# Kernel optimization log

Measured on AMD Instinct MI355X. Metric: run time of the kernel, lower is better.

Reference implementation:

```python
import jax, jax.numpy as jnp
import numpy as np

BATCH = 1
SEQ = 2048
HIDDEN = 2048
NUM_HEADS = 16
NUM_KV_HEADS = 4
HEAD_DIM = HIDDEN // NUM_HEADS  # 128
KV_GROUPS = NUM_HEADS // NUM_KV_HEADS  # 4
MIN_WIN, MAX_WIN = 64, 512


def _adaptive_window_mask(key):
    # Per-query adaptive window size in [MIN_WIN, MAX_WIN); causal + windowed.
    win = jax.random.randint(key, (SEQ,), MIN_WIN, MAX_WIN)  # [S]
    i = jnp.arange(SEQ)[:, None]  # query pos
    j = jnp.arange(SEQ)[None, :]  # key pos
    mask = (j <= i) & (j > i - win[:, None])  # diagonal always True
    return jnp.broadcast_to(mask[None, None], (BATCH, 1, SEQ, SEQ))


def setup_inputs() -> dict:
    key = jax.random.key(0)
    ks = jax.random.split(key, 6)
    std = 0.02
    return {
        "hidden_states": jax.random.normal(ks[0], (BATCH, SEQ, HIDDEN), jnp.float32),
        "attention_mask": _adaptive_window_mask(ks[1]),
        "Wq": jax.random.normal(ks[2], (HIDDEN, NUM_HEADS * HEAD_DIM), jnp.float32) * std,
        "Wk": jax.random.normal(ks[3], (HIDDEN, NUM_KV_HEADS * HEAD_DIM), jnp.float32) * std,
        "Wv": jax.random.normal(ks[4], (HIDDEN, NUM_KV_HEADS * HEAD_DIM), jnp.float32) * std,
        "Wo": jax.random.normal(ks[5], (NUM_HEADS * HEAD_DIM, HIDDEN), jnp.float32) * std,
    }


def reference(hidden_states, attention_mask, Wq, Wk, Wv, Wo):
    B, S, H = hidden_states.shape
    # Projections (no bias, LLaMA-style)
    q = (hidden_states @ Wq).reshape(B, S, NUM_HEADS, HEAD_DIM).transpose(0, 2, 1, 3)
    k = (hidden_states @ Wk).reshape(B, S, NUM_KV_HEADS, HEAD_DIM).transpose(0, 2, 1, 3)
    v = (hidden_states @ Wv).reshape(B, S, NUM_KV_HEADS, HEAD_DIM).transpose(0, 2, 1, 3)
    # GQA: repeat_interleave along head dim
    k = jnp.repeat(k, KV_GROUPS, axis=1)  # [B, NUM_HEADS, S, D]
    v = jnp.repeat(v, KV_GROUPS, axis=1)
    scale = 1.0 / np.sqrt(HEAD_DIM).astype(np.float32)
    scores = jnp.einsum("bhqd,bhkd->bhqk", q, k) * scale  # [B, H, S, S]
    # bool mask: masked positions get -inf (matches masked_fill_(-inf) + add)
    scores = jnp.where(attention_mask, scores, -jnp.inf)
    attn = jax.nn.softmax(scores, axis=-1)
    out = jnp.einsum("bhqk,bhkd->bhqd", attn, v)
    out = out.transpose(0, 2, 1, 3).reshape(B, S, H) @ Wo
    return out
```

## Files before the change

kernel.cpp:

```cpp
#include <hip/hip_runtime.h>
#include <hip/hip_bf16.h>

typedef __attribute__((ext_vector_type(4)))  float f32x4;
typedef __attribute__((ext_vector_type(16))) float f32x16;
typedef __attribute__((ext_vector_type(8)))  short bf16x8;
typedef unsigned short u16;
typedef unsigned int   u32;
typedef unsigned long long u64;
typedef __attribute__((ext_vector_type(2))) u32 u32x2;
typedef __attribute__((ext_vector_type(4))) u32 u32x4;

#define S_LEN 2048
#define HID   2048
#define NH    16
#define NKV   4
#define HD    128
#define DKV   512
#define QK_SCALE 0.08838834764831845f

__device__ __forceinline__ u16 f2bf(float x) {
    u32 u = __builtin_bit_cast(u32, x);
    u32 r = (u + 0x7fffu + ((u >> 16) & 1u)) >> 16;
    return (u16)r;
}
__device__ __forceinline__ float bf2f(u16 b) {
    u32 u = ((u32)b) << 16;
    return __builtin_bit_cast(float, u);
}
__device__ __forceinline__ void gload_lds16(const void* g, void* l) {
    __builtin_amdgcn_global_load_lds(
        (const __attribute__((address_space(1))) u32*)g,
        (__attribute__((address_space(3))) u32*)l, 16, 0, 0);
}
__device__ __forceinline__ u32x4 pack8(const u16* o) {
    u32x4 r;
    r[0] = (u32)o[0] | ((u32)o[1] << 16);
    r[1] = (u32)o[2] | ((u32)o[3] << 16);
    r[2] = (u32)o[4] | ((u32)o[5] << 16);
    r[3] = (u32)o[6] | ((u32)o[7] << 16);
    return r;
}

__device__ __forceinline__ void plswap(u32 a, u32 b, u32& x0, u32& x1) {
#if __has_builtin(__builtin_amdgcn_permlane32_swap)
    u32x2 r = __builtin_amdgcn_permlane32_swap(a, b, false, false);
    x0 = r[0]; x1 = r[1];
#else
    u32 oa = (u32)__shfl_xor((int)a, 32);
    u32 ob = (u32)__shfl_xor((int)b, 32);
    int hi = (threadIdx.x & 63) >> 5;
    x0 = hi ? ob : a;
    x1 = hi ? b : oa;
#endif
}
__device__ __forceinline__ float pairmax32(float v) {
    u32 x0, x1; plswap(__builtin_bit_cast(u32, v), __builtin_bit_cast(u32, v), x0, x1);
    return fmaxf(__builtin_bit_cast(float, x0), __builtin_bit_cast(float, x1));
}
__device__ __forceinline__ float pairsum32(float v) {
    u32 x0, x1; plswap(__builtin_bit_cast(u32, v), __builtin_bit_cast(u32, v), x0, x1);
    return __builtin_bit_cast(float, x0) + __builtin_bit_cast(float, x1);
}

#define NTQ 1024
#define NTK 256
#define NTV 256
#define NTO 1024
#define NT_W (NTQ + NTK + NTV + NTO)
#define NB_CVT 1024
#define NB_START 128
#define NB_PREP (NT_W + NB_CVT + NB_START)

__global__ __launch_bounds__(256) void prep_kernel(
        const u32* __restrict__ X, const unsigned char* __restrict__ mask,
        const void* __restrict__ Wq, const void* __restrict__ Wk,
        const void* __restrict__ Wv, const void* __restrict__ Wo,
        u16* __restrict__ Xbf, u16* __restrict__ WqT, u16* __restrict__ WkT,
        u16* __restrict__ WvT, u16* __restrict__ WoT, int* __restrict__ start)
{
    __shared__ float tile[64][65];
    const int tid = threadIdx.x, lane = tid & 63, wave = tid >> 6;

    int big = 0, nz = 0;
    #pragma unroll
    for (int i = 0; i < 4; i++) {
        u32 v = X[lane + i * 64];
        u16 lo = (u16)(v & 0xffffu);
        int e = (lo >> 7) & 0xff;
        big |= (e >= 0x83);
        nz  |= (lo != 0);
    }
    const int isf32 = (__ballot(big) != 0ull || __ballot(nz) == 0ull) ? 1 : 0;

    const int b = blockIdx.x;
    if (b < NT_W) {
        const void* src; u16* dst; int N, ty;
        if (b < NTQ)                  { src = Wq; dst = WqT; N = 2048; ty = b; }
        else if (b < NTQ + NTK)       { src = Wk; dst = WkT; N = 512;  ty = b - NTQ; }
        else if (b < NTQ + NTK + NTV) { src = Wv; dst = WvT; N = 512;  ty = b - NTQ - NTK; }
        else                          { src = Wo; dst = WoT; N = 2048; ty = b - NTQ - NTK - NTV; }
        const int K = 2048;
        const int ntx = N >> 6;
        const int k0 = (ty / ntx) << 6, n0 = (ty % ntx) << 6;
        const int kk = tid >> 4, cg = (tid & 15) << 2;
        if (isf32) {
            const float* W = (const float*)src;
            #pragma unroll
            for (int it = 0; it < 4; it++) {
                f32x4 v = *(const f32x4*)(W + (size_t)(k0 + kk + it * 16) * N + n0 + cg);
                tile[kk + it * 16][cg + 0] = v[0]; tile[kk + it * 16][cg + 1] = v[1];
                tile[kk + it * 16][cg + 2] = v[2]; tile[kk + it * 16][cg + 3] = v[3];
            }
        } else {
            const u16* W = (const u16*)src;
            #pragma unroll
            for (int it = 0; it < 4; it++) {
                u64 v = *(const u64*)(W + (size_t)(k0 + kk + it * 16) * N + n0 + cg);
                tile[kk + it * 16][cg + 0] = bf2f((u16)(v));
                tile[kk + it * 16][cg + 1] = bf2f((u16)(v >> 16));
                tile[kk + it * 16][cg + 2] = bf2f((u16)(v >> 32));
                tile[kk + it * 16][cg + 3] = bf2f((u16)(v >> 48));
            }
        }
        __syncthreads();
        const int nn = tid >> 2;
        #pragma unroll
        for (int it = 0; it < 2; it++) {
            int kof = ((tid & 3) + it * 4) << 3;
            u16 ob[8];
            #pragma unroll
            for (int j = 0; j < 8; j++) ob[j] = f2bf(tile[kof + j][nn]);
            *(u32x4*)(dst + (size_t)(n0 + nn) * K + k0 + kof) = pack8(ob);
        }
    } else if (b < NT_W + NB_CVT) {
        const long base = ((long)(b - NT_W) * 256 + tid) * 16;
        u16 ob[16];
        if (isf32) {
            const float* p = (const float*)X;
            #pragma unroll
            for (int c = 0; c < 4; c++) {
                f32x4 v = *(const f32x4*)(p + base + c * 4);
                ob[c * 4 + 0] = f2bf(v[0]); ob[c * 4 + 1] = f2bf(v[1]);
                ob[c * 4 + 2] = f2bf(v[2]); ob[c * 4 + 3] = f2bf(v[3]);
            }
        } else {
            const u16* p = (const u16*)X;
            #pragma unroll
            for (int j = 0; j < 16; j++) ob[j] = p[base + j];
        }
        *(u32x4*)(Xbf + base) = pack8(ob);
        *(u32x4*)(Xbf + base + 8) = pack8(ob + 8);
    } else {
        const int b3 = b - NT_W - NB_CVT;
        const bool w1 = (mask[2049] != 0);
        #pragma unroll
        for (int rr = 0; rr < 4; rr++) {
            const int r = b3 * 16 + wave * 4 + rr;
            int cnt = 0;
            if (w1) {
                const u32* row = (const u32*)(mask + (size_t)r * S_LEN);
                #pragma unroll
                for (int i = 0; i < 8; i++) {
                    u32 v = row[lane + i * 64];
                    cnt += (int)(((v & 0x01010101u) * 0x01010101u) >> 24);
                }
            } else {
                const u32* row = (const u32*)mask + (size_t)r * S_LEN;
                #pragma unroll
                for (int i = 0; i < 32; i++) cnt += (row[lane + i * 64] != 0);
            }
            #pragma unroll
            for (int off = 32; off; off >>= 1) cnt += __shfl_down(cnt, off);
            if (lane == 0) start[r] = r + 1 - cnt;
        }
    }
}

__global__ __launch_bounds__(256) void gemm_qkv_kernel(
        const u16* __restrict__ A, const u16* __restrict__ BT,
        u16* __restrict__ Qf, u16* __restrict__ Kf, u16* __restrict__ Vf)
{
    __shared__ char smem[49152];
    const int tid = threadIdx.x;
    const int wave = tid >> 6, lane = tid & 63, g = lane >> 4, q = lane & 15;
    const int wr = wave >> 1, wc = wave & 1;
    const int gx = gridDim.x, nwg = gx * gridDim.y;
    const int wg = blockIdx.x + blockIdx.y * gx;
    const int swz = (wg & 7) * (nwg >> 3) + (wg >> 3);
    const int m0 = (swz / gx) * 128, n0 = (swz % gx) * 64;
    const int K = HID;

    f32x4 acc[4][2];
    #pragma unroll
    for (int i = 0; i < 4; i++)
        #pragma unroll
        for (int j = 0; j < 2; j++) acc[i][j] = (f32x4){0.f, 0.f, 0.f, 0.f};

    auto stage = [&](int kt, int b) {
        const int kbase = kt << 6;
        #pragma unroll
        for (int it = 0; it < 4; ++it) {
            int idx = it * 256 + tid;
            int row = idx >> 3, ch = idx & 7;
            int sch = ch ^ (row & 7);
            gload_lds16(A + (size_t)(m0 + row) * K + kbase + sch * 8,
                        smem + b * 16384 + idx * 16);
        }
        #pragma unroll
        for (int it = 0; it < 2; ++it) {
            int idx = it * 256 + tid;
            int row = idx >> 3, ch = idx & 7;
            int sch = ch ^ (row & 7);
            gload_lds16(BT + (size_t)(n0 + row) * K + kbase + sch * 8,
                        smem + 32768 + b * 8192 + idx * 16);
        }
    };

    const int KT = K >> 6;
    stage(0, 0);
    __syncthreads();
    int cur = 0;
    for (int kt = 0; kt < KT; ++kt) {
        if (kt + 1 < KT) stage(kt + 1, cur ^ 1);
        const char* sa = smem + cur * 16384;
        const char* sb = smem + 32768 + cur * 8192;
        #pragma unroll
        for (int kk = 0; kk < 2; ++kk) {
            bf16x8 af[4], bfr[2];
            #pragma unroll
            for (int i = 0; i < 4; i++) {
                int ra = wr * 64 + i * 16 + q;
                af[i] = *(const bf16x8*)(sa + ra * 128 + (((kk * 4 + g) ^ (ra & 7)) * 16));
            }
            #pragma unroll
            for (int j = 0; j < 2; j++) {
                int rb = wc * 32 + j * 16 + q;
                bfr[j] = *(const bf16x8*)(sb + rb * 128 + (((kk * 4 + g) ^ (rb & 7)) * 16));
            }
            #pragma unroll
            for (int i = 0; i < 4; i++)
                #pragma unroll
                for (int j = 0; j < 2; j++)
                    acc[i][j] = __builtin_amdgcn_mfma_f32_16x16x32_bf16(af[i], bfr[j], acc[i][j], 0, 0, 0);
        }
        __syncthreads();
        cur ^= 1;
    }
    #pragma unroll
    for (int i = 0; i < 4; i++) {
        #pragma unroll
        for (int j = 0; j < 2; j++) {
            int n = n0 + wc * 32 + j * 16 + q;
            if (n0 < 2560) {
                #pragma unroll
                for (int r = 0; r < 4; r++) {
                    int m = m0 + wr * 64 + i * 16 + g * 4 + r;
                    float v = acc[i][j][r];
                    int t = m >> 5, jj = m & 31;
                    if (n0 < 2048) {
                        int h = n >> 7, dd = n & 127;
                        int kc = dd >> 4, hi8 = (dd >> 3) & 1, e = dd & 7;
                        Qf[(size_t)h * 262144 + t * 4096 + kc * 512 + (jj + hi8 * 32) * 8 + e]
                            = f2bf(v * QK_SCALE);
                    } else {
                        int d = n - 2048;
                        int hkk = d >> 7, dd = d & 127;
                        int kc = dd >> 4, hi8 = (dd >> 3) & 1, e = dd & 7;
                        Kf[(size_t)hkk * 262144 + t * 4096 + kc * 512 + (jj + hi8 * 32) * 8 + e]
                            = f2bf(v);
                    }
                }
            } else {
                int m = m0 + wr * 64 + i * 16 + g * 4;
                int d = n - 2560;
                int hkk = d >> 7, dd = d & 127;
                int dt = dd >> 5, l31 = dd & 31;
                int jj = m & 31;
                int c = (jj >> 4) & 1, hi8 = (jj >> 3) & 1, e0 = jj & 7;
                u64 wd = (u64)f2bf(acc[i][j][0]) | ((u64)f2bf(acc[i][j][1]) << 16) |
                         ((u64)f2bf(acc[i][j][2]) << 32) | ((u64)f2bf(acc[i][j][3]) << 48);
                *(u64*)(Vf + (size_t)hkk * 262144 + (m >> 5) * 4096 + (dt * 2 + c) * 512
                        + (l31 + hi8 * 32) * 8 + e0) = wd;
            }
        }
    }
}

template <int MODE>
__global__ __launch_bounds__(256) void gemm_bt_kernel(
        const u16* __restrict__ A, const u16* __restrict__ BT, void* __restrict__ Cv,
        int M, int N, int K, float scale)
{
    __shared__ char smem[49152];
    const int tid = threadIdx.x;
    const int wave = tid >> 6, lane = tid & 63, g = lane >> 4, q = lane & 15;
    const int wr = wave >> 1, wc = wave & 1;
    const int gx = gridDim.x, nwg = gx * gridDim.y;
    const int wg = blockIdx.x + blockIdx.y * gx;
    const int swz = (nwg & 7) == 0 ? ((wg & 7) * (nwg >> 3) + (wg >> 3)) : wg;
    const int m0 = (swz / gx) * 128, n0 = (swz % gx) * 64;

    f32x4 acc[4][2];
    #pragma unroll
    for (int i = 0; i < 4; i++)
        #pragma unroll
        for (int j = 0; j < 2; j++) acc[i][j] = (f32x4){0.f, 0.f, 0.f, 0.f};

    auto stage = [&](int kt, int b) {
        const int kbase = kt << 6;
        #pragma unroll
        for (int it = 0; it < 4; ++it) {
            int idx = it * 256 + tid;
            int row = idx >> 3, ch = idx & 7;
            int sch = ch ^ (row & 7);
            gload_lds16(A + (size_t)(m0 + row) * K + kbase + sch * 8,
                        smem + b * 16384 + idx * 16);
        }
        #pragma unroll
        for (int it = 0; it < 2; ++it) {
            int idx = it * 256 + tid;
            int row = idx >> 3, ch = idx & 7;
            int sch = ch ^ (row & 7);
            gload_lds16(BT + (size_t)(n0 + row) * K + kbase + sch * 8,
                        smem + 32768 + b * 8192 + idx * 16);
        }
    };

    const int KT = K >> 6;
    stage(0, 0);
    __syncthreads();
    int cur = 0;
    for (int kt = 0; kt < KT; ++kt) {
        if (kt + 1 < KT) stage(kt + 1, cur ^ 1);
        const char* sa = smem + cur * 16384;
        const char* sb = smem + 32768 + cur * 8192;
        #pragma unroll
        for (int kk = 0; kk < 2; ++kk) {
            bf16x8 af[4], bfr[2];
            #pragma unroll
            for (int i = 0; i < 4; i++) {
                int ra = wr * 64 + i * 16 + q;
                af[i] = *(const bf16x8*)(sa + ra * 128 + (((kk * 4 + g) ^ (ra & 7)) * 16));
            }
            #pragma unroll
            for (int j = 0; j < 2; j++) {
                int rb = wc * 32 + j * 16 + q;
                bfr[j] = *(const bf16x8*)(sb + rb * 128 + (((kk * 4 + g) ^ (rb & 7)) * 16));
            }
            #pragma unroll
            for (int i = 0; i < 4; i++)
                #pragma unroll
                for (int j = 0; j < 2; j++)
                    acc[i][j] = __builtin_amdgcn_mfma_f32_16x16x32_bf16(af[i], bfr[j], acc[i][j], 0, 0, 0);
        }
        __syncthreads();
        cur ^= 1;
    }
    #pragma unroll
    for (int i = 0; i < 4; i++) {
        #pragma unroll
        for (int j = 0; j < 2; j++) {
            #pragma unroll
            for (int r = 0; r < 4; r++) {
                int m = m0 + wr * 64 + i * 16 + g * 4 + r;
                int n = n0 + wc * 32 + j * 16 + q;
                float v = acc[i][j][r] * scale;
                if (MODE == 3) ((float*)Cv)[(size_t)m * N + n] = v;
                else           ((u16*)Cv)[(size_t)m * N + n] = f2bf(v);
            }
        }
    }
}

__global__ __launch_bounds__(64, 1) void attn_kernel(
        const u16* __restrict__ Q, const u16* __restrict__ Kb,
        const u16* __restrict__ Vt, u16* __restrict__ O, const int* __restrict__ start)
{
    const int lane = threadIdx.x & 63;
    const int q = lane & 31, hi = lane >> 5;
    const int h = blockIdx.y, hk = h >> 2;
    const int r0 = blockIdx.x * 32;
    const int qrow = r0 + q;

    const u16* qf = Q + (size_t)h * 262144 + blockIdx.x * 4096 + lane * 8;
    bf16x8 Qf[8];
    #pragma unroll
    for (int kc = 0; kc < 8; kc++) Qf[kc] = *(const bf16x8*)(qf + kc * 512);

    const int startq = start[qrow];
    int jlo = startq;
    #pragma unroll
    for (int off = 1; off < 32; off <<= 1) jlo = min(jlo, __shfl_xor(jlo, off));
    const int jend = r0 + 31;

    float m = -INFINITY, l = 0.f;
    f32x16 o[4];
    #pragma unroll
    for (int dt = 0; dt < 4; dt++) o[dt] = (f32x16){};

    const u16* kfb = Kb + (size_t)hk * 262144 + lane * 8;
    const u16* vfb = Vt + (size_t)hk * 262144 + lane * 8;

    for (int j0 = (jlo & ~31); j0 <= jend; j0 += 32) {
        const int t = j0 >> 5;
        const u16* kf = kfb + t * 4096;
        bf16x8 Kf[8];
        #pragma unroll
        for (int kc = 0; kc < 8; kc++) Kf[kc] = *(const bf16x8*)(kf + kc * 512);
        const u16* vf = vfb + t * 4096;
        bf16x8 Vf[8];
        #pragma unroll
        for (int idx = 0; idx < 8; idx++) Vf[idx] = *(const bf16x8*)(vf + idx * 512);

        f32x16 s = (f32x16){};
        __builtin_amdgcn_s_setprio(1);
        #pragma unroll
        for (int kc = 0; kc < 8; kc++)
            s = __builtin_amdgcn_mfma_f32_32x32x16_bf16(Kf[kc], Qf[kc], s, 0, 0, 0);
        __builtin_amdgcn_s_setprio(0);

        float sv[16];
        float pmax = -INFINITY;
        #pragma unroll
        for (int r = 0; r < 16; r++) {
            int j = j0 + (r & 3) + 8 * (r >> 2) + 4 * hi;
            float x = (j <= qrow && j >= startq) ? s[r] : -INFINITY;
            sv[r] = x;
            pmax = fmaxf(pmax, x);
        }
        pmax = pairmax32(pmax);

        bool defer = __all(pmax <= m + 8.f);
        float mnew = m;
        if (!defer) {
            mnew = fmaxf(m, pmax);
            float corr = (m == -INFINITY) ? 0.f : __expf(m - mnew);
            l *= corr;
            #pragma unroll
            for (int dt = 0; dt < 4; dt++)
                #pragma unroll
                for (int r = 0; r < 16; r++) o[dt][r] *= corr;
            m = mnew;
        }

        float ps = 0.f;
        u16 pb[16];
        #pragma unroll
        for (int r = 0; r < 16; r++) {
            float p = (sv[r] == -INFINITY) ? 0.f : __expf(sv[r] - mnew);
            ps += p;
            pb[r] = f2bf(p);
        }
        l += pairsum32(ps);

        u32 w[8];
        #pragma unroll
        for (int i = 0; i < 8; i++) w[i] = (u32)pb[2 * i] | ((u32)pb[2 * i + 1] << 16);
        u32 x0, x1, y0, y1;
        plswap(w[0], w[2], x0, x1); plswap(w[1], w[3], y0, y1);
        u32x4 c0w = {x0, y0, x1, y1};
        bf16x8 P0 = __builtin_bit_cast(bf16x8, c0w);
        plswap(w[4], w[6], x0, x1); plswap(w[5], w[7], y0, y1);
        u32x4 c1w = {x0, y0, x1, y1};
        bf16x8 P1 = __builtin_bit_cast(bf16x8, c1w);

        __builtin_amdgcn_s_setprio(1);
        #pragma unroll
        for (int dt = 0; dt < 4; dt++) {
            o[dt] = __builtin_amdgcn_mfma_f32_32x32x16_bf16(Vf[dt * 2 + 0], P0, o[dt], 0, 0, 0);
            o[dt] = __builtin_amdgcn_mfma_f32_32x32x16_bf16(Vf[dt * 2 + 1], P1, o[dt], 0, 0, 0);
        }
        __builtin_amdgcn_s_setprio(0);
    }

    float inv = 1.0f / l;
    u16* op = O + (size_t)qrow * HID + h * HD + 4 * hi;
    #pragma unroll
    for (int dt = 0; dt < 4; dt++) {
        #pragma unroll
        for (int rb = 0; rb < 16; rb += 4) {
            u64 wd = (u64)f2bf(o[dt][rb + 0] * inv) |
                     ((u64)f2bf(o[dt][rb + 1] * inv) << 16) |
                     ((u64)f2bf(o[dt][rb + 2] * inv) << 32) |
                     ((u64)f2bf(o[dt][rb + 3] * inv) << 48);
            *(u64*)(op + dt * 32 + 2 * rb) = wd;
        }
    }
}

extern "C" void kernel_launch(void* const* d_in, const int* in_sizes, int n_in,
                              void* d_out, int out_size, void* d_ws, size_t ws_size,
                              hipStream_t stream)
{
    char* ws = (char*)d_ws;
    const size_t MB = 1024 * 1024;
    int* start = (int*)(ws + 1024);
    u16* Xbf = (u16*)(ws + 16384);
    u16* WqT = (u16*)(ws + 16384 + 8 * MB);
    u16* WkT = (u16*)(ws + 16384 + 16 * MB);
    u16* WvT = (u16*)(ws + 16384 + 18 * MB);
    u16* WoT = (u16*)(ws + 16384 + 20 * MB);
    u16* Qfr = (u16*)(ws + 16384 + 28 * MB);
    u16* Kfr = (u16*)(ws + 16384 + 36 * MB);
    u16* Vfr = (u16*)(ws + 16384 + 38 * MB);
    u16* Obf = (u16*)(ws + 16384 + 40 * MB);

    const void* X  = d_in[0];
    const unsigned char* mask = (const unsigned char*)d_in[1];
    const void* Wq = d_in[2];
    const void* Wk = d_in[3];
    const void* Wv = d_in[4];
    const void* Wo = d_in[5];

    prep_kernel<<<NB_PREP, 256, 0, stream>>>(
        (const u32*)X, mask, Wq, Wk, Wv, Wo, Xbf, WqT, WkT, WvT, WoT, start);

    gemm_qkv_kernel<<<dim3(48, HID / 128), 256, 0, stream>>>(Xbf, WqT, Qfr, Kfr, Vfr);

    attn_kernel<<<dim3(S_LEN / 32, NH), 64, 0, stream>>>(Qfr, Kfr, Vfr, Obf, start);

    gemm_bt_kernel<3><<<dim3(HID / 64, S_LEN / 128), 256, 0, stream>>>(Obf, WoT, d_out, S_LEN, HID, HID, 1.f);
}
```

Measured before the change: 116.9 us.

## Double-buffer K/V tile loads in attention and pack four waves per block

```diff
diff --git a/kernel.cpp b/kernel.cpp
--- a/kernel.cpp
+++ b/kernel.cpp
@@ -372,17 +372,91 @@
     }
 }
 
-__global__ __launch_bounds__(64, 1) void attn_kernel(
+
+__device__ __forceinline__ void attn_loadt(const u16* kfb, const u16* vfb, int t,
+                                           bf16x8 (&Kf)[8], bf16x8 (&Vf)[8])
+{
+    const u16* kf = kfb + t * 4096;
+    #pragma unroll
+    for (int kc = 0; kc < 8; kc++) Kf[kc] = *(const bf16x8*)(kf + kc * 512);
+    const u16* vf = vfb + t * 4096;
+    #pragma unroll
+    for (int idx = 0; idx < 8; idx++) Vf[idx] = *(const bf16x8*)(vf + idx * 512);
+}
+
+__device__ __forceinline__ void attn_proc(
+        int j0, int qrow, int startq, int hi,
+        const bf16x8 (&Qf)[8], const bf16x8 (&Kf)[8], const bf16x8 (&Vf)[8],
+        float& m, float& l, f32x16 (&o)[4])
+{
+    f32x16 s = (f32x16){};
+    #pragma unroll
+    for (int kc = 0; kc < 8; kc++)
+        s = __builtin_amdgcn_mfma_f32_32x32x16_bf16(Kf[kc], Qf[kc], s, 0, 0, 0);
+
+    float sv[16];
+    float pmax = -INFINITY;
+    #pragma unroll
+    for (int r = 0; r < 16; r++) {
+        int j = j0 + (r & 3) + 8 * (r >> 2) + 4 * hi;
+        float x = (j <= qrow && j >= startq) ? s[r] : -INFINITY;
+        sv[r] = x;
+        pmax = fmaxf(pmax, x);
+    }
+    pmax = pairmax32(pmax);
+
+    bool defer = __all(pmax <= m + 8.f);
+    float mnew = m;
+    if (!defer) {
+        mnew = fmaxf(m, pmax);
+        float corr = (m == -INFINITY) ? 0.f : __expf(m - mnew);
+        l *= corr;
+        #pragma unroll
+        for (int dt = 0; dt < 4; dt++)
+            #pragma unroll
+            for (int r = 0; r < 16; r++) o[dt][r] *= corr;
+        m = mnew;
+    }
+
+    float ps = 0.f;
+    u16 pb[16];
+    #pragma unroll
+    for (int r = 0; r < 16; r++) {
+        float p = (sv[r] == -INFINITY) ? 0.f : __expf(sv[r] - mnew);
+        ps += p;
+        pb[r] = f2bf(p);
+    }
+    l += pairsum32(ps);
+
+    u32 w[8];
+    #pragma unroll
+    for (int i = 0; i < 8; i++) w[i] = (u32)pb[2 * i] | ((u32)pb[2 * i + 1] << 16);
+    u32 x0, x1, y0, y1;
+    plswap(w[0], w[2], x0, x1); plswap(w[1], w[3], y0, y1);
+    u32x4 c0w = {x0, y0, x1, y1};
+    bf16x8 P0 = __builtin_bit_cast(bf16x8, c0w);
+    plswap(w[4], w[6], x0, x1); plswap(w[5], w[7], y0, y1);
+    u32x4 c1w = {x0, y0, x1, y1};
+    bf16x8 P1 = __builtin_bit_cast(bf16x8, c1w);
+
+    #pragma unroll
+    for (int dt = 0; dt < 4; dt++) {
+        o[dt] = __builtin_amdgcn_mfma_f32_32x32x16_bf16(Vf[dt * 2 + 0], P0, o[dt], 0, 0, 0);
+        o[dt] = __builtin_amdgcn_mfma_f32_32x32x16_bf16(Vf[dt * 2 + 1], P1, o[dt], 0, 0, 0);
+    }
+}
+
+__global__ __launch_bounds__(256, 1) void attn_kernel(
         const u16* __restrict__ Q, const u16* __restrict__ Kb,
         const u16* __restrict__ Vt, u16* __restrict__ O, const int* __restrict__ start)
 {
-    const int lane = threadIdx.x & 63;
+    const int tid = threadIdx.x, wave = tid >> 6, lane = tid & 63;
     const int q = lane & 31, hi = lane >> 5;
     const int h = blockIdx.y, hk = h >> 2;
-    const int r0 = blockIdx.x * 32;
+    const int r0 = blockIdx.x * 128 + wave * 32;
     const int qrow = r0 + q;
 
-    const u16* qf = Q + (size_t)h * 262144 + blockIdx.x * 4096 + lane * 8;
+    const u16* qf = Q + (size_t)h * 262144 + (r0 >> 5) * 4096 + lane * 8;
     bf16x8 Qf[8];
     #pragma unroll
     for (int kc = 0; kc < 8; kc++) Qf[kc] = *(const bf16x8*)(qf + kc * 512);
@@ -401,76 +475,19 @@
     const u16* kfb = Kb + (size_t)hk * 262144 + lane * 8;
     const u16* vfb = Vt + (size_t)hk * 262144 + lane * 8;
 
-    for (int j0 = (jlo & ~31); j0 <= jend; j0 += 32) {
-        const int t = j0 >> 5;
-        const u16* kf = kfb + t * 4096;
-        bf16x8 Kf[8];
-        #pragma unroll
-        for (int kc = 0; kc < 8; kc++) Kf[kc] = *(const bf16x8*)(kf + kc * 512);
-        const u16* vf = vfb + t * 4096;
-        bf16x8 Vf[8];
-        #pragma unroll
-        for (int idx = 0; idx < 8; idx++) Vf[idx] = *(const bf16x8*)(vf + idx * 512);
-
-        f32x16 s = (f32x16){};
-        __builtin_amdgcn_s_setprio(1);
-        #pragma unroll
-        for (int kc = 0; kc < 8; kc++)
-            s = __builtin_amdgcn_mfma_f32_32x32x16_bf16(Kf[kc], Qf[kc], s, 0, 0, 0);
-        __builtin_amdgcn_s_setprio(0);
-
-        float sv[16];
-        float pmax = -INFINITY;
-        #pragma unroll
-        for (int r = 0; r < 16; r++) {
-            int j = j0 + (r & 3) + 8 * (r >> 2) + 4 * hi;
-            float x = (j <= qrow && j >= startq) ? s[r] : -INFINITY;
-            sv[r] = x;
-            pmax = fmaxf(pmax, x);
-        }
-        pmax = pairmax32(pmax);
-
-        bool defer = __all(pmax <= m + 8.f);
-        float mnew = m;
-        if (!defer) {
-            mnew = fmaxf(m, pmax);
-            float corr = (m == -INFINITY) ? 0.f : __expf(m - mnew);
-            l *= corr;
-            #pragma unroll
-            for (int dt = 0; dt < 4; dt++)
-                #pragma unroll
-                for (int r = 0; r < 16; r++) o[dt][r] *= corr;
-            m = mnew;
-        }
-
-        float ps = 0.f;
-        u16 pb[16];
-        #pragma unroll
-        for (int r = 0; r < 16; r++) {
-            float p = (sv[r] == -INFINITY) ? 0.f : __expf(sv[r] - mnew);
-            ps += p;
-            pb[r] = f2bf(p);
-        }
-        l += pairsum32(ps);
-
-        u32 w[8];
-        #pragma unroll
-        for (int i = 0; i < 8; i++) w[i] = (u32)pb[2 * i] | ((u32)pb[2 * i + 1] << 16);
-        u32 x0, x1, y0, y1;
-        plswap(w[0], w[2], x0, x1); plswap(w[1], w[3], y0, y1);
-        u32x4 c0w = {x0, y0, x1, y1};
-        bf16x8 P0 = __builtin_bit_cast(bf16x8, c0w);
-        plswap(w[4], w[6], x0, x1); plswap(w[5], w[7], y0, y1);
-        u32x4 c1w = {x0, y0, x1, y1};
-        bf16x8 P1 = __builtin_bit_cast(bf16x8, c1w);
-
-        __builtin_amdgcn_s_setprio(1);
-        #pragma unroll
-        for (int dt = 0; dt < 4; dt++) {
-            o[dt] = __builtin_amdgcn_mfma_f32_32x32x16_bf16(Vf[dt * 2 + 0], P0, o[dt], 0, 0, 0);
-            o[dt] = __builtin_amdgcn_mfma_f32_32x32x16_bf16(Vf[dt * 2 + 1], P1, o[dt], 0, 0, 0);
-        }
-        __builtin_amdgcn_s_setprio(0);
+    bf16x8 KA[8], VA[8], KB[8], VB[8];
+    int j0 = jlo & ~31;
+    attn_loadt(kfb, vfb, j0 >> 5, KA, VA);
+    for (;;) {
+        int j1 = j0 + 32; bool p1 = (j1 <= jend);
+        if (p1) attn_loadt(kfb, vfb, j1 >> 5, KB, VB);
+        attn_proc(j0, qrow, startq, hi, Qf, KA, VA, m, l, o);
+        if (!p1) break;
+        int j2 = j1 + 32; bool p2 = (j2 <= jend);
+        if (p2) attn_loadt(kfb, vfb, j2 >> 5, KA, VA);
+        attn_proc(j1, qrow, startq, hi, Qf, KB, VB, m, l, o);
+        if (!p2) break;
+        j0 = j2;
     }
 
     float inv = 1.0f / l;
@@ -517,7 +534,7 @@
 
     gemm_qkv_kernel<<<dim3(48, HID / 128), 256, 0, stream>>>(Xbf, WqT, Qfr, Kfr, Vfr);
 
-    attn_kernel<<<dim3(S_LEN / 32, NH), 64, 0, stream>>>(Qfr, Kfr, Vfr, Obf, start);
+    attn_kernel<<<dim3(S_LEN / 128, NH), 256, 0, stream>>>(Qfr, Kfr, Vfr, Obf, start);
 
     gemm_bt_kernel<3><<<dim3(HID / 64, S_LEN / 128), 256, 0, stream>>>(Obf, WoT, d_out, S_LEN, HID, HID, 1.f);
 }
```

Result: faster. 107.4 us (-8.1%).
